# Optimization experiments

Measured on AMD Instinct MI355X. Metric: run time of the kernel, lower is better.

## Reference

```python
import jax, jax.numpy as jnp
import numpy as np

INPUT_DIM, HIDDEN, LATENT = 17, 512, 256
B, T = 4096, 512


def setup_inputs() -> dict:
    key = jax.random.key(0)
    ks = jax.random.split(key, 16)
    s = 0.02
    inp = {
        "x": jax.random.normal(ks[0], (B, T, INPUT_DIM), dtype=jnp.float32),
        "h0": jnp.zeros((B, HIDDEN), dtype=jnp.float32),
        # encoder: Linear(17->256), ReLU, Linear(256->256), ReLU
        "enc_w1": jax.random.normal(ks[1], (LATENT, INPUT_DIM)) * s,
        "enc_b1": jnp.zeros((LATENT,), jnp.float32),
        "enc_w2": jax.random.normal(ks[2], (LATENT, LATENT)) * s,
        "enc_b2": jnp.zeros((LATENT,), jnp.float32),
        # GRUCell(latent+1 -> hidden): gates ordered [r, z, n] as in torch
        "w_ih": jax.random.normal(ks[3], (3 * HIDDEN, LATENT + 1)) * s,
        "w_hh": jax.random.normal(ks[4], (3 * HIDDEN, HIDDEN)) * s,
        "b_ih": jnp.zeros((3 * HIDDEN,), jnp.float32),
        "b_hh": jnp.zeros((3 * HIDDEN,), jnp.float32),
        "q_w": jax.random.normal(ks[5], (4, HIDDEN)) * s,
        "q_b": jnp.zeros((4,), jnp.float32),
        "v_w": jax.random.normal(ks[6], (3, HIDDEN)) * s,
        "v_b": jnp.zeros((3,), jnp.float32),
        "c_w": jax.random.normal(ks[7], (3, HIDDEN)) * s,
        "c_b": jnp.zeros((3,), jnp.float32),
    }
    return inp


def _quat_to_rotmat(q):
    # q: [B, 4] = [w, x, y, z] -> R: [B, 3, 3]
    w, x, y, z = q[:, 0], q[:, 1], q[:, 2], q[:, 3]
    xx, yy, zz = x * x, y * y, z * z
    xy, xz, yz = x * y, x * z, y * z
    wx, wy, wz = w * x, w * y, w * z
    r0 = jnp.stack([1 - 2 * (yy + zz), 2 * (xy - wz), 2 * (xz + wy)], axis=-1)
    r1 = jnp.stack([2 * (xy + wz), 1 - 2 * (xx + zz), 2 * (yz - wx)], axis=-1)
    r2 = jnp.stack([2 * (xz - wy), 2 * (yz + wx), 1 - 2 * (xx + yy)], axis=-1)
    return jnp.stack([r0, r1, r2], axis=1)


def _gru_cell(xin, h, w_ih, w_hh, b_ih, b_hh):
    gi = xin @ w_ih.T + b_ih  # [B, 3H]
    gh = h @ w_hh.T + b_hh
    i_r, i_z, i_n = jnp.split(gi, 3, axis=-1)
    h_r, h_z, h_n = jnp.split(gh, 3, axis=-1)
    r = jax.nn.sigmoid(i_r + h_r)
    z = jax.nn.sigmoid(i_z + h_z)
    n = jnp.tanh(i_n + r * h_n)
    return (1.0 - z) * n + z * h


def _forward(x, h0, enc_w1, enc_b1, enc_w2, enc_b2, w_ih, w_hh, b_ih, b_hh,
             q_w, q_b, v_w, v_b, c_w, c_b):
    xt = jnp.swapaxes(x, 0, 1)  # [T, B, 17]

    def step(carry, x_t):
        h, dp = carry
        dt = x_t[:, -1:]                      # [B, 1]
        acc = x_t[:, 0:3]                     # [B, 3]
        z1 = jax.nn.relu(x_t @ enc_w1.T + enc_b1)
        lat = jax.nn.relu(z1 @ enc_w2.T + enc_b2)
        gin = jnp.concatenate([lat, dt], axis=-1)
        h = _gru_cell(gin, h, w_ih, w_hh, b_ih, b_hh)
        q_raw = h @ q_w.T + q_b
        # F.normalize(p=2, eps=1e-12)
        q = q_raw / jnp.maximum(jnp.linalg.norm(q_raw, axis=-1, keepdims=True), 1e-12)
        v_world = h @ v_w.T + v_b
        R = _quat_to_rotmat(q)
        acc_world = jnp.einsum('bij,bj->bi', R, acc)
        dp_baseline = v_world * dt + 0.5 * acc_world * dt * dt
        eps = h @ c_w.T + c_b
        dp = dp + dp_baseline + eps
        return (h, dp), None

    total_dp0 = jnp.zeros((x.shape[0], 3), dtype=x.dtype)
    (h_f, total_dp), _ = jax.lax.scan(step, (h0, total_dp0), xt)
    return total_dp


def reference(x, h0, enc_w1, enc_b1, enc_w2, enc_b2, w_ih, w_hh, b_ih, b_hh,
              q_w, q_b, v_w, v_b, c_w, c_b):
    return _forward(x, h0, enc_w1, enc_b1, enc_w2, enc_b2, w_ih, w_hh, b_ih,
                    b_hh, q_w, q_b, v_w, v_b, c_w, c_b)
```

## Files before the change

kernel.cpp:

```cpp
#include <hip/hip_runtime.h>
#include <math.h>

#define T_STEPS 512
#define IN_DIM  17
#define HID     512
#define LAT     256
#define BT      16
#define NTH     512
#define CHUNK   4

typedef __attribute__((ext_vector_type(8))) _Float16 half8;
typedef __attribute__((ext_vector_type(4))) float    f32x4;

#define OFF_HB0   0
#define OFF_HB1   4194304
#define OFF_LAT   8388608
#define OFF_WG    16777216
#define OFF_W2P   19136512
#define OFF_W1P   19267584
#define OFF_HEADP 19283968
#define OFF_W256  19300352
#define OFF_BCOMB 19306496
#define OFF_BHN   19312640
#define OFF_DT    19314688
#define OFF_CTR   19380224

static __device__ inline unsigned short f2h(float f) {
    union { _Float16 h; unsigned short u; } cv;
    cv.h = (_Float16)f;
    return cv.u;
}

__global__ void pack_kernel(const float* __restrict__ enc_w1,
                            const float* __restrict__ enc_w2,
                            const float* __restrict__ w_ih,
                            const float* __restrict__ w_hh,
                            const float* __restrict__ b_ih,
                            const float* __restrict__ b_hh,
                            const float* __restrict__ q_w,
                            const float* __restrict__ v_w,
                            const float* __restrict__ c_w,
                            const float* __restrict__ h0,
                            unsigned char* __restrict__ ws) {
    unsigned short* wgP   = (unsigned short*)(ws + OFF_WG);
    unsigned short* w2P   = (unsigned short*)(ws + OFF_W2P);
    unsigned short* w1P   = (unsigned short*)(ws + OFF_W1P);
    unsigned short* headP = (unsigned short*)(ws + OFF_HEADP);
    unsigned short* hb0   = (unsigned short*)(ws + OFF_HB0);
    float* w256  = (float*)(ws + OFF_W256);
    float* bcomb = (float*)(ws + OFF_BCOMB);
    float* bhn   = (float*)(ws + OFF_BHN);
    unsigned int* ctr = (unsigned int*)(ws + OFF_CTR);

    const int tid = blockIdx.x * blockDim.x + threadIdx.x;
    const int stride = gridDim.x * blockDim.x;

    for (int idx = tid; idx < 32 * 24 * 3 * 64 * 8; idx += stride) {
        int j = idx & 7, l = (idx >> 3) & 63;
        int r = idx >> 9;
        int g = r % 3; r /= 3;
        int kt = r % 24; int s = r / 24;
        int row = g * 512 + s * 16 + (l & 15);
        int kk  = ((l >> 4) & 3) * 8 + j;
        float v;
        if (kt < 8) v = w_ih[(size_t)row * 257 + (kt * 32 + kk)];
        else        v = w_hh[(size_t)row * 512 + ((kt - 8) * 32 + kk)];
        wgP[idx] = f2h(v);
    }
    for (int idx = tid; idx < 16 * 8 * 64 * 8; idx += stride) {
        int j = idx & 7, l = (idx >> 3) & 63, kt = (idx >> 9) & 7, nt = idx >> 12;
        int n = nt * 16 + (l & 15);
        int k = kt * 32 + ((l >> 4) & 3) * 8 + j;
        w2P[idx] = f2h(enc_w2[(size_t)n * 256 + k]);
    }
    for (int idx = tid; idx < 16 * 64 * 8; idx += stride) {
        int j = idx & 7, l = (idx >> 3) & 63, nt = idx >> 9;
        int n = nt * 16 + (l & 15);
        int k = ((l >> 4) & 3) * 8 + j;
        w1P[idx] = (k < IN_DIM) ? f2h(enc_w1[(size_t)n * IN_DIM + k]) : (unsigned short)0;
    }
    for (int idx = tid; idx < 16 * 64 * 8; idx += stride) {
        int j = idx & 7, l = (idx >> 3) & 63, kt = idx >> 9;
        int d = l & 15;
        int k = kt * 32 + ((l >> 4) & 3) * 8 + j;
        float v = 0.f;
        if (d < 4)       v = q_w[(size_t)d * HID + k];
        else if (d < 7)  v = v_w[(size_t)(d - 4) * HID + k];
        else if (d < 10) v = c_w[(size_t)(d - 7) * HID + k];
        headP[idx] = f2h(v);
    }
    for (int idx = tid; idx < 1536; idx += stride) {
        w256[idx]  = w_ih[(size_t)idx * 257 + 256];
        bcomb[idx] = (idx < 1024) ? (b_ih[idx] + b_hh[idx]) : b_ih[idx];
    }
    for (int idx = tid; idx < 512; idx += stride) bhn[idx] = b_hh[1024 + idx];
    for (int idx = tid; idx < 4096 * 512; idx += stride) {
        int c  = idx & 15;
        int r  = (idx >> 4) & 511;
        int sg = idx >> 13;
        int gg = sg >> 5, ss = sg & 31;
        hb0[idx] = f2h(h0[((size_t)(gg * 512 + r)) * 512 + ss * 16 + c]);
    }
    for (int idx = tid; idx < 4096; idx += stride) ctr[idx] = 0;
}

#define MFMA16(a, b, c) __builtin_amdgcn_mfma_f32_16x16x32_f16((a), (b), (c), 0, 0, 0)

static __device__ inline void tag_arrive(unsigned int* slot, int ss, unsigned int tag) {
    __syncthreads();
    if (threadIdx.x == 0)
        __hip_atomic_store(slot + ss, tag, __ATOMIC_RELAXED, __HIP_MEMORY_SCOPE_AGENT);
}
static __device__ inline void tag_wait(unsigned int* slot, unsigned int tag) {
    if (threadIdx.x < 32) {
        const int lane = (int)threadIdx.x;
        unsigned int spins = 0;
        while (__hip_atomic_load(slot + lane, __ATOMIC_RELAXED, __HIP_MEMORY_SCOPE_AGENT) < tag) {
            __builtin_amdgcn_s_sleep(1);
            if (++spins > 50000000u) break;
        }
    }
    __syncthreads();
    asm volatile("buffer_inv sc0" ::: "memory");
}

__global__ __launch_bounds__(NTH, 2)
void imu_coop_kernel(const float* __restrict__ x,
                     const float* __restrict__ h0,
                     const float* __restrict__ enc_b1,
                     const float* __restrict__ enc_b2,
                     const float* __restrict__ q_b,
                     const float* __restrict__ v_b,
                     const float* __restrict__ c_b,
                     unsigned char* __restrict__ ws,
                     float* __restrict__ out)
{
    __shared__ __align__(16) unsigned short wgL[24 * 3 * 64 * 8];
    __shared__ __align__(16) unsigned short headL[16 * 64 * 8];
    __shared__ __align__(16) unsigned short xbf64[64][32];
    __shared__ __align__(16) unsigned short z1bf64[64][264];
    __shared__ __align__(16) float          sdotP[8][16][17];
    __shared__ float eb1L[256], eb2L[256];
    __shared__ float dtL[512][4];
    __shared__ float xownL[2][4][16][4];
    __shared__ float sdS[16][10];
    __shared__ int   s_slS;

    unsigned short* hb[2] = { (unsigned short*)(ws + OFF_HB0),
                              (unsigned short*)(ws + OFF_HB1) };
    unsigned short*       latbuf = (unsigned short*)(ws + OFF_LAT);
    const unsigned short* wgP    = (const unsigned short*)(ws + OFF_WG);
    const unsigned short* w2P    = (const unsigned short*)(ws + OFF_W2P);
    const unsigned short* w1P    = (const unsigned short*)(ws + OFF_W1P);
    const unsigned short* headP  = (const unsigned short*)(ws + OFF_HEADP);
    const float* w256g = (const float*)(ws + OFF_W256);
    const float* bcmg  = (const float*)(ws + OFF_BCOMB);
    const float* bhng  = (const float*)(ws + OFF_BHN);
    float* dtbuf = (float*)(ws + OFF_DT);

    const int t    = threadIdx.x;
    const int w    = t >> 6;
    const int l    = t & 63;
    const int l15  = l & 15;
    const int lq   = (l >> 4) & 3;
    const int lqh  = lq >> 1;
    const int c8   = (lq & 1) * 8;

    unsigned int xcc;
    asm volatile("s_getreg_b32 %0, hwreg(HW_REG_XCC_ID)" : "=s"(xcc));
    const int g = (int)(xcc & 7u);
    if (t == 0) {
        unsigned int* tk = (unsigned int*)(ws + OFF_CTR) + 2048 + g;
        s_slS = (int)(__hip_atomic_fetch_add(tk, 1u, __ATOMIC_RELAXED,
                                             __HIP_MEMORY_SCOPE_AGENT) & 31u);
    }
    __syncthreads();
    const int s_sl = s_slS;
    const int eb0  = g * 512 + s_sl * 16;

    unsigned int* stepslot  = (unsigned int*)(ws + OFF_CTR) + (size_t)g * 32;
    unsigned int* chunkslot = (unsigned int*)(ws + OFF_CTR + 4096) + (size_t)g * 32;

    const f32x4 fz = {0.f, 0.f, 0.f, 0.f};

    {
        const uint4* src = (const uint4*)(wgP + (size_t)s_sl * (24 * 3 * 64 * 8));
        uint4* dst = (uint4*)wgL;
        for (int i = t; i < 24 * 3 * 64; i += NTH) dst[i] = src[i];
    }
    {
        const uint4* src = (const uint4*)headP;
        uint4* dst = (uint4*)headL;
        for (int i = t; i < 16 * 64; i += NTH) dst[i] = src[i];
    }
    for (int idx = t; idx < 256; idx += NTH) { eb1L[idx] = enc_b1[idx]; eb2L[idx] = enc_b2[idx]; }
    for (int idx = t; idx < 64 * 32; idx += NTH) xbf64[idx >> 5][idx & 31] = 0;

    const float qb0 = q_b[0], qb1 = q_b[1], qb2 = q_b[2], qb3 = q_b[3];
    const float vb0 = v_b[0], vb1 = v_b[1], vb2 = v_b[2];
    const float cb0 = c_b[0], cb1 = c_b[1], cb2 = c_b[2];

    const int jd = s_sl * 16 + l15;
    const float bR  = bcmg[jd],        bZ  = bcmg[512 + jd];
    const float bIN = bcmg[1024 + jd], bHN = bhng[jd];
    const float wr2 = w256g[jd], wz2 = w256g[512 + jd], wn2 = w256g[1024 + jd];

    float ho[4][4];
    #pragma unroll
    for (int mt = 0; mt < 4; ++mt)
        #pragma unroll
        for (int i = 0; i < 4; ++i)
            ho[mt][i] = h0[(size_t)(g * 512 + w * 64 + mt * 16 + lq * 4 + i) * HID + jd];

    float dp0 = 0.f, dp1 = 0.f, dp2 = 0.f;
    f32x4 eReg[4][2];
    __syncthreads();

    const size_t r0 = (size_t)(g * 512 + w * 64) + l15;

#define STAGE_CHUNK(cchunk)                                                          \
  { const int c_ = (cchunk);                                                         \
    for (int idx = t; idx < 17 * 16 * CHUNK; idx += NTH) {                           \
        int k = idx % 17, rem = idx / 17;                                            \
        int b = rem & 15, cc = rem >> 4;                                             \
        float v = x[((size_t)(eb0 + b) * T_STEPS + (c_ * 4 + cc)) * IN_DIM + k];     \
        xbf64[cc * 16 + b][k] = f2h(v);                                              \
        if (k < 3) xownL[c_ & 1][cc][b][k] = v;                                      \
        if (k == 16) {                                                               \
            dtbuf[(size_t)(eb0 + b) * 4 + cc] = v;                                   \
            xownL[c_ & 1][cc][b][3] = v;                                             \
        }                                                                            \
    }                                                                                \
    __syncthreads();                                                                 \
    { const int nt0 = 2 * w, nt1 = 2 * w + 1;                                        \
      half8 bv0 = *(const half8*)(w1P + ((size_t)nt0 * 64 + l) * 8);                 \
      half8 bv1 = *(const half8*)(w1P + ((size_t)nt1 * 64 + l) * 8);                 \
      f32x4 e1[4][2];                                                                \
      _Pragma("unroll")                                                              \
      for (int mt = 0; mt < 4; ++mt) {                                               \
          half8 av = *(const half8*)&xbf64[mt * 16 + l15][lq * 8];                   \
          e1[mt][0] = MFMA16(av, bv0, fz);                                           \
          e1[mt][1] = MFMA16(av, bv1, fz);                                           \
      }                                                                              \
      __syncthreads();                                                               \
      _Pragma("unroll")                                                              \
      for (int mt = 0; mt < 4; ++mt)                                                 \
          _Pragma("unroll")                                                          \
          for (int i = 0; i < 4; ++i) {                                              \
              int m64 = mt * 16 + lq * 4 + i;                                        \
              int n0 = nt0 * 16 + l15, n1 = nt1 * 16 + l15;                          \
              z1bf64[m64][n0] = f2h(fmaxf(e1[mt][0][i] + eb1L[n0], 0.f));            \
              z1bf64[m64][n1] = f2h(fmaxf(e1[mt][1][i] + eb1L[n1], 0.f));            \
          }                                                                          \
    }                                                                                \
    __syncthreads();                                                                 \
    { const int nt0 = 2 * w, nt1 = 2 * w + 1;                                        \
      _Pragma("unroll")                                                              \
      for (int mt = 0; mt < 4; ++mt) { eReg[mt][0] = fz; eReg[mt][1] = fz; }         \
      _Pragma("unroll")                                                              \
      for (int kt = 0; kt < 8; ++kt) {                                               \
          half8 bv0 = *(const half8*)(w2P + ((size_t)(nt0 * 8 + kt) * 64 + l) * 8);  \
          half8 bv1 = *(const half8*)(w2P + ((size_t)(nt1 * 8 + kt) * 64 + l) * 8);  \
          _Pragma("unroll")                                                          \
          for (int mt = 0; mt < 4; ++mt) {                                           \
              half8 av = *(const half8*)&z1bf64[mt * 16 + l15][kt * 32 + lq * 8];    \
              eReg[mt][0] = MFMA16(av, bv0, eReg[mt][0]);                            \
              eReg[mt][1] = MFMA16(av, bv1, eReg[mt][1]);                            \
          }                                                                          \
      }                                                                              \
    }                                                                                \
  }

#define LATWRITE()                                                                   \
  { const int nt0 = 2 * w, nt1 = 2 * w + 1;                                          \
    _Pragma("unroll")                                                                \
    for (int mt = 0; mt < 4; ++mt)                                                   \
        _Pragma("unroll")                                                            \
        for (int i = 0; i < 4; ++i) {                                                \
            int b = lq * 4 + i;                                                      \
            int n0 = nt0 * 16 + l15, n1 = nt1 * 16 + l15;                            \
            size_t rb = ((size_t)(eb0 + b) * 4 + mt) * 256;                          \
            latbuf[rb + n0] = f2h(fmaxf(eReg[mt][0][i] + eb2L[n0], 0.f));            \
            latbuf[rb + n1] = f2h(fmaxf(eReg[mt][1][i] + eb2L[n1], 0.f));            \
        } }

#define LDA_L(dst, ktv)                                                         \
            { _Pragma("unroll")                                                 \
              for (int mt = 0; mt < 4; ++mt)                                    \
                  dst[mt] = *(const half8*)(latp + (size_t)mt * (16 * 4 * 256) + (ktv) * 32); }
#define LDA_H(dst, ktv)                                                         \
            { _Pragma("unroll")                                                 \
              for (int mt = 0; mt < 4; ++mt)                                    \
                  dst[mt] = *(const half8*)(hA + (size_t)((ktv) - 8) * 16384 + mt * 256); }
#define LDB(dst, ktv)                                                           \
            { _Pragma("unroll")                                                 \
              for (int gg = 0; gg < 3; ++gg)                                    \
                  dst[gg] = *(const half8*)&wgL[(((ktv) * 3 + gg) * 64 + l) * 8]; }
#define DOMF_L(A, B)                                                            \
            { _Pragma("unroll")                                                 \
              for (int mt = 0; mt < 4; ++mt) {                                  \
                  aR[mt]  = MFMA16(A[mt], B[0], aR[mt]);                        \
                  aZ[mt]  = MFMA16(A[mt], B[1], aZ[mt]);                        \
                  aNi[mt] = MFMA16(A[mt], B[2], aNi[mt]); } }
#define DOMF_H(A, B)                                                            \
            { _Pragma("unroll")                                                 \
              for (int mt = 0; mt < 4; ++mt) {                                  \
                  aR[mt]  = MFMA16(A[mt], B[0], aR[mt]);                        \
                  aZ[mt]  = MFMA16(A[mt], B[1], aZ[mt]);                        \
                  aNh[mt] = MFMA16(A[mt], B[2], aNh[mt]); } }

    STAGE_CHUNK(0);
    LATWRITE();
    tag_arrive(chunkslot, s_sl, 1u);
    tag_wait(chunkslot, 1u);
    {
        const float* srcdt = dtbuf + (size_t)g * 2048;
        float* dstdt = &dtL[0][0];
        for (int idx = t; idx < 2048; idx += NTH) dstdt[idx] = srcdt[idx];
    }
    __syncthreads();

    for (int s = 0; s < T_STEPS; ++s) {
        const int cs = s & 3;
        const int rp = s & 1, wp = rp ^ 1;
        const unsigned short* hgx = hb[rp] + (size_t)g * 262144;
        unsigned short*       hwx = hb[wp] + (size_t)g * 262144 + (size_t)s_sl * 8192;

        if (cs == 0 && s > 0) {
            const int c = s >> 2;
            tag_wait(stepslot, (unsigned int)s);
            LATWRITE();
            tag_arrive(chunkslot, s_sl, (unsigned int)(c + 1));
            tag_wait(chunkslot, (unsigned int)(c + 1));
            {
                const float* srcdt = dtbuf + (size_t)g * 2048;
                float* dstdt = &dtL[0][0];
                for (int idx = t; idx < 2048; idx += NTH) dstdt[idx] = srcdt[idx];
            }
            __syncthreads();
        }

        f32x4 aR[4], aZ[4], aNi[4], aNh[4];
        #pragma unroll
        for (int mt = 0; mt < 4; ++mt) { aR[mt] = fz; aZ[mt] = fz; aNi[mt] = fz; aNh[mt] = fz; }

        {
            const unsigned short* latp = latbuf + (r0 * 4 + cs) * 256 + lq * 8;
            half8 aF[3][4], bF[2][3];
            LDA_L(aF[0], 0); LDA_L(aF[1], 1); LDA_L(aF[2], 2);
            LDB(bF[0], 0); LDB(bF[1], 1);
            #pragma unroll
            for (int kt = 0; kt < 8; ++kt) {
                DOMF_L(aF[kt % 3], bF[kt & 1]);
                if (kt < 5) LDA_L(aF[kt % 3], kt + 3);
                if (kt < 6) LDB(bF[kt & 1], kt + 2);
            }
        }

        if (cs != 0 && s > 0) tag_wait(stepslot, (unsigned int)s);

        const unsigned short* hA = hgx + (size_t)lqh * 8192
                                       + (size_t)(w * 64 + l15) * 16 + c8;
        half8 aH[4][4], bH[2][3];
        LDA_H(aH[0], 8); LDA_H(aH[1], 9); LDA_H(aH[2], 10); LDA_H(aH[3], 11);
        LDB(bH[0], 8); LDB(bH[1], 9);

        if (s > 0) {
            f32x4 hc = fz;
            const int ka = 2 * w, kb = 2 * w + 1;
            const unsigned short* hH = hgx + (size_t)(s_sl * 16 + l15) * 16 + c8;
            half8 a0 = *(const half8*)(hH + (size_t)(2 * ka + lqh) * 8192);
            half8 b0 = *(const half8*)(headL + ((size_t)ka * 64 + l) * 8);
            half8 a1 = *(const half8*)(hH + (size_t)(2 * kb + lqh) * 8192);
            half8 b1 = *(const half8*)(headL + ((size_t)kb * 64 + l) * 8);
            hc = MFMA16(a0, b0, hc);
            hc = MFMA16(a1, b1, hc);
            #pragma unroll
            for (int i = 0; i < 4; ++i) sdotP[w][lq * 4 + i][l15] = hc[i];
            __syncthreads();
            if (t < 160) {
                const int b = t / 10, d = t % 10;
                float acc = 0.f;
                #pragma unroll
                for (int w8 = 0; w8 < 8; ++w8) acc += sdotP[w8][b][d];
                sdS[b][d] = acc;
            }
            __syncthreads();
            if (t < BT) {
                const int b = t;
                const int ps = s - 1, pcc = ps & 3, ppar = (ps >> 2) & 1;
                float ax = xownL[ppar][pcc][b][0], ay = xownL[ppar][pcc][b][1];
                float az = xownL[ppar][pcc][b][2], dtv = xownL[ppar][pcc][b][3];
                float q0 = sdS[b][0] + qb0, q1 = sdS[b][1] + qb1;
                float q2 = sdS[b][2] + qb2, q3 = sdS[b][3] + qb3;
                float nrm = fmaxf(sqrtf(q0*q0 + q1*q1 + q2*q2 + q3*q3), 1e-12f);
                float qw = q0/nrm, qx = q1/nrm, qy = q2/nrm, qz = q3/nrm;
                float vx = sdS[b][4] + vb0, vy = sdS[b][5] + vb1, vz = sdS[b][6] + vb2;
                float ex = sdS[b][7] + cb0, ey = sdS[b][8] + cb1, ez = sdS[b][9] + cb2;
                float xx = qx*qx, yy = qy*qy, zz = qz*qz;
                float xy = qx*qy, xz = qx*qz, yz = qy*qz;
                float wxq = qw*qx, wyq = qw*qy, wzq = qw*qz;
                float aw0 = (1.f - 2.f*(yy+zz))*ax + 2.f*(xy-wzq)*ay + 2.f*(xz+wyq)*az;
                float aw1 = 2.f*(xy+wzq)*ax + (1.f - 2.f*(xx+zz))*ay + 2.f*(yz-wxq)*az;
                float aw2 = 2.f*(xz-wyq)*ax + 2.f*(yz+wxq)*ay + (1.f - 2.f*(xx+yy))*az;
                float hdt2 = 0.5f * dtv * dtv;
                dp0 += vx*dtv + aw0*hdt2 + ex;
                dp1 += vy*dtv + aw1*hdt2 + ey;
                dp2 += vz*dtv + aw2*hdt2 + ez;
            }
        }

        #pragma unroll
        for (int k2 = 0; k2 < 16; ++k2) {
            DOMF_H(aH[k2 & 3], bH[k2 & 1]);
            if (k2 < 12) LDA_H(aH[k2 & 3], k2 + 12);
            if (k2 < 14) LDB(bH[k2 & 1], k2 + 10);
        }

        #pragma unroll
        for (int mt = 0; mt < 4; ++mt) {
            #pragma unroll
            for (int i = 0; i < 4; ++i) {
                const int rl = w * 64 + mt * 16 + lq * 4 + i;
                float dtv = dtL[rl][cs];
                float gr = aR[mt][i]  + bR  + dtv * wr2;
                float gz = aZ[mt][i]  + bZ  + dtv * wz2;
                float gi = aNi[mt][i] + bIN + dtv * wn2;
                float gh = aNh[mt][i] + bHN;
                float r  = 1.f / (1.f + __expf(-gr));
                float zg = 1.f / (1.f + __expf(-gz));
                float narg = gi + r * gh;
                float n  = 1.f - 2.f / (__expf(2.f * narg) + 1.f);
                float hn = (1.f - zg) * n + zg * ho[mt][i];
                ho[mt][i] = hn;
                hwx[rl * 16 + l15] = f2h(hn);
            }
        }
        tag_arrive(stepslot, s_sl, (unsigned int)(s + 1));

        if (cs == 3) {
            const int c = s >> 2;
            if (c + 1 < T_STEPS / CHUNK) STAGE_CHUNK(c + 1);
        }
    }
#undef LDA_L
#undef LDA_H
#undef LDB
#undef DOMF_L
#undef DOMF_H

    tag_wait(stepslot, (unsigned int)T_STEPS);
    {
        const unsigned short* hgx = hb[T_STEPS & 1] + (size_t)g * 262144;
        f32x4 hc = fz;
        const int ka = 2 * w, kb = 2 * w + 1;
        const unsigned short* hH = hgx + (size_t)(s_sl * 16 + l15) * 16 + c8;
        half8 a0 = *(const half8*)(hH + (size_t)(2 * ka + lqh) * 8192);
        half8 b0 = *(const half8*)(headL + ((size_t)ka * 64 + l) * 8);
        half8 a1 = *(const half8*)(hH + (size_t)(2 * kb + lqh) * 8192);
        half8 b1 = *(const half8*)(headL + ((size_t)kb * 64 + l) * 8);
        hc = MFMA16(a0, b0, hc);
        hc = MFMA16(a1, b1, hc);
        #pragma unroll
        for (int i = 0; i < 4; ++i) sdotP[w][lq * 4 + i][l15] = hc[i];
    }
    __syncthreads();
    if (t < BT) {
        const int b = t;
        float sd[10];
        #pragma unroll
        for (int d = 0; d < 10; ++d) {
            float acc = 0.f;
            #pragma unroll
            for (int w8 = 0; w8 < 8; ++w8) acc += sdotP[w8][b][d];
            sd[d] = acc;
        }
        const int pcc = (T_STEPS - 1) & 3, ppar = ((T_STEPS - 1) >> 2) & 1;
        float ax = xownL[ppar][pcc][b][0], ay = xownL[ppar][pcc][b][1];
        float az = xownL[ppar][pcc][b][2], dtv = xownL[ppar][pcc][b][3];
        float q0 = sd[0] + qb0, q1 = sd[1] + qb1;
        float q2 = sd[2] + qb2, q3 = sd[3] + qb3;
        float nrm = fmaxf(sqrtf(q0*q0 + q1*q1 + q2*q2 + q3*q3), 1e-12f);
        float qw = q0/nrm, qx = q1/nrm, qy = q2/nrm, qz = q3/nrm;
        float vx = sd[4] + vb0, vy = sd[5] + vb1, vz = sd[6] + vb2;
        float ex = sd[7] + cb0, ey = sd[8] + cb1, ez = sd[9] + cb2;
        float xx = qx*qx, yy = qy*qy, zz = qz*qz;
        float xy = qx*qy, xz = qx*qz, yz = qy*qz;
        float wxq = qw*qx, wyq = qw*qy, wzq = qw*qz;
        float aw0 = (1.f - 2.f*(yy+zz))*ax + 2.f*(xy-wzq)*ay + 2.f*(xz+wyq)*az;
        float aw1 = 2.f*(xy+wzq)*ax + (1.f - 2.f*(xx+zz))*ay + 2.f*(yz-wxq)*az;
        float aw2 = 2.f*(xz-wyq)*ax + 2.f*(yz+wxq)*ay + (1.f - 2.f*(xx+yy))*az;
        float hdt2 = 0.5f * dtv * dtv;
        dp0 += vx*dtv + aw0*hdt2 + ex;
        dp1 += vy*dtv + aw1*hdt2 + ey;
        dp2 += vz*dtv + aw2*hdt2 + ez;
        out[(size_t)(eb0 + b) * 3 + 0] = dp0;
        out[(size_t)(eb0 + b) * 3 + 1] = dp1;
        out[(size_t)(eb0 + b) * 3 + 2] = dp2;
    }
}

extern "C" void kernel_launch(void* const* d_in, const int* in_sizes, int n_in,
                              void* d_out, int out_size, void* d_ws, size_t ws_size,
                              hipStream_t stream) {
    const float* x      = (const float*)d_in[0];
    const float* h0     = (const float*)d_in[1];
    const float* enc_w1 = (const float*)d_in[2];
    const float* enc_b1 = (const float*)d_in[3];
    const float* enc_w2 = (const float*)d_in[4];
    const float* enc_b2 = (const float*)d_in[5];
    const float* w_ih   = (const float*)d_in[6];
    const float* w_hh   = (const float*)d_in[7];
    const float* b_ih   = (const float*)d_in[8];
    const float* b_hh   = (const float*)d_in[9];
    const float* q_w    = (const float*)d_in[10];
    const float* q_b    = (const float*)d_in[11];
    const float* v_w    = (const float*)d_in[12];
    const float* v_b    = (const float*)d_in[13];
    const float* c_w    = (const float*)d_in[14];
    const float* c_b    = (const float*)d_in[15];
    unsigned char* ws = (unsigned char*)d_ws;
    float* out = (float*)d_out;

    hipLaunchKernelGGL(pack_kernel, dim3(2048), dim3(256), 0, stream,
                       enc_w1, enc_w2, w_ih, w_hh, b_ih, b_hh, q_w, v_w, c_w, h0, ws);

    void* args[] = { (void*)&x, (void*)&h0, (void*)&enc_b1, (void*)&enc_b2,
                     (void*)&q_b, (void*)&v_b, (void*)&c_b, (void*)&ws, (void*)&out };
    (void)hipLaunchCooperativeKernel((void*)imu_coop_kernel, dim3(256), dim3(NTH),
                                     args, 0, stream);
}
```

Measured before the change: 12.77 ms.

## Replace per-step global barrier with fine-grained per-slice waits in GRU recurrence

```diff
diff --git a/kernel.cpp b/kernel.cpp
--- a/kernel.cpp
+++ b/kernel.cpp
@@ -122,6 +122,20 @@
     }
     __syncthreads();
     asm volatile("buffer_inv sc0" ::: "memory");
+}
+
+static __device__ inline void slot_wait2(const unsigned int* slot, int ss0,
+                                         unsigned int tag, bool* dead) {
+    if (*dead) return;
+    const unsigned int* p = slot + ss0 + (int)(threadIdx.x & 1);
+    unsigned int spins = 0;
+    while (true) {
+        unsigned int v = __hip_atomic_load(p, __ATOMIC_RELAXED, __HIP_MEMORY_SCOPE_AGENT);
+        if (__all(v >= tag)) break;
+        __builtin_amdgcn_s_sleep(1);
+        if (++spins > 1000000u) { *dead = true; break; }
+    }
+    asm volatile("" ::: "memory");
 }
 
 __global__ __launch_bounds__(NTH, 2)
@@ -214,6 +228,7 @@
 
     float dp0 = 0.f, dp1 = 0.f, dp2 = 0.f;
     f32x4 eReg[4][2];
+    bool dead = false;
     __syncthreads();
 
     const size_t r0 = (size_t)(g * 512 + w * 64) + l15;
@@ -291,7 +306,7 @@
 #define LDA_H(dst, ktv)                                                         \
             { _Pragma("unroll")                                                 \
               for (int mt = 0; mt < 4; ++mt)                                    \
-                  dst[mt] = *(const half8*)(hA + (size_t)((ktv) - 8) * 16384 + mt * 256); }
+                  dst[mt] = *(const half8*)(hA + (size_t)(ktv) * 16384 + mt * 256); }
 #define LDB(dst, ktv)                                                           \
             { _Pragma("unroll")                                                 \
               for (int gg = 0; gg < 3; ++gg)                                    \
@@ -357,13 +372,51 @@
             }
         }
 
-        if (cs != 0 && s > 0) tag_wait(stepslot, (unsigned int)s);
-
-        const unsigned short* hA = hgx + (size_t)lqh * 8192
-                                       + (size_t)(w * 64 + l15) * 16 + c8;
-        half8 aH[4][4], bH[2][3];
-        LDA_H(aH[0], 8); LDA_H(aH[1], 9); LDA_H(aH[2], 10); LDA_H(aH[3], 11);
-        LDB(bH[0], 8); LDB(bH[1], 9);
+        asm volatile("buffer_inv sc0" ::: "memory");
+        {
+            const unsigned short* hA = hgx + (size_t)lqh * 8192
+                                           + (size_t)(w * 64 + l15) * 16 + c8;
+            const int kt0 = s_sl >> 1;
+            half8 aH[2][4], bH[2][3];
+            {
+                int ka = kt0 & 15;
+                slot_wait2(stepslot, 2 * ka, (unsigned int)s, &dead);
+                LDA_H(aH[0], ka); LDB(bH[0], ka + 8);
+                int kb = (kt0 + 1) & 15;
+                slot_wait2(stepslot, 2 * kb, (unsigned int)s, &dead);
+                LDA_H(aH[1], kb); LDB(bH[1], kb + 8);
+            }
+            for (int j = 0; j < 16; ++j) {
+                const int cur = j & 1;
+                int kn = 0;
+                if (j < 14) {
+                    kn = (kt0 + j + 2) & 15;
+                    slot_wait2(stepslot, 2 * kn, (unsigned int)s, &dead);
+                }
+                DOMF_H(aH[cur], bH[cur]);
+                if (j < 14) { LDA_H(aH[cur], kn); LDB(bH[cur], kn + 8); }
+            }
+        }
+
+        #pragma unroll
+        for (int mt = 0; mt < 4; ++mt) {
+            #pragma unroll
+            for (int i = 0; i < 4; ++i) {
+                const int rl = w * 64 + mt * 16 + lq * 4 + i;
+                float dtv = dtL[rl][cs];
+                float gr = aR[mt][i]  + bR  + dtv * wr2;
+                float gz = aZ[mt][i]  + bZ  + dtv * wz2;
+                float gi = aNi[mt][i] + bIN + dtv * wn2;
+                float gh = aNh[mt][i] + bHN;
+                float r  = 1.f / (1.f + __expf(-gr));
+                float zg = 1.f / (1.f + __expf(-gz));
+                float narg = gi + r * gh;
+                float n  = 1.f - 2.f / (__expf(2.f * narg) + 1.f);
+                float hn = (1.f - zg) * n + zg * ho[mt][i];
+                ho[mt][i] = hn;
+                hwx[rl * 16 + l15] = f2h(hn);
+            }
+        }
 
         if (s > 0) {
             f32x4 hc = fz;
@@ -410,32 +463,6 @@
             }
         }
 
-        #pragma unroll
-        for (int k2 = 0; k2 < 16; ++k2) {
-            DOMF_H(aH[k2 & 3], bH[k2 & 1]);
-            if (k2 < 12) LDA_H(aH[k2 & 3], k2 + 12);
-            if (k2 < 14) LDB(bH[k2 & 1], k2 + 10);
-        }
-
-        #pragma unroll
-        for (int mt = 0; mt < 4; ++mt) {
-            #pragma unroll
-            for (int i = 0; i < 4; ++i) {
-                const int rl = w * 64 + mt * 16 + lq * 4 + i;
-                float dtv = dtL[rl][cs];
-                float gr = aR[mt][i]  + bR  + dtv * wr2;
-                float gz = aZ[mt][i]  + bZ  + dtv * wz2;
-                float gi = aNi[mt][i] + bIN + dtv * wn2;
-                float gh = aNh[mt][i] + bHN;
-                float r  = 1.f / (1.f + __expf(-gr));
-                float zg = 1.f / (1.f + __expf(-gz));
-                float narg = gi + r * gh;
-                float n  = 1.f - 2.f / (__expf(2.f * narg) + 1.f);
-                float hn = (1.f - zg) * n + zg * ho[mt][i];
-                ho[mt][i] = hn;
-                hwx[rl * 16 + l15] = f2h(hn);
-            }
-        }
         tag_arrive(stepslot, s_sl, (unsigned int)(s + 1));
 
         if (cs == 3) {
```

New measurement: 13.73 ms. 1.08x slower.
